# Performance work log

Hardware: AMD Instinct MI355X
Metric: run time of the kernel (lower is better)

Reference implementation:

```python
import jax, jax.numpy as jnp
import numpy as np


def _dplr_scan(q, k, v, a, b, gk, scale=1.0):
    """RWKV-7 DPLR delta-rule recurrence. All inputs [B,H,S,D]; fp32 state."""
    B, H, S, D = q.shape
    Dv = v.shape[-1]
    h0 = jnp.zeros((B, H, D, Dv), dtype=jnp.float32)
    qf = q.astype(jnp.float32) * scale
    kf = k.astype(jnp.float32)
    vf = v.astype(jnp.float32)
    af = a.astype(jnp.float32)
    bf = b.astype(jnp.float32)
    gf = gk.astype(jnp.float32)

    def step(h, xs):
        q_t, k_t, v_t, a_t, b_t, gk_t = xs  # each [B,H,D]
        a_h = jnp.einsum('bhk,bhkv->bhv', a_t, h)
        h = jnp.exp(gk_t)[..., None] * h + b_t[..., None] * a_h[..., None, :] \
            + jnp.einsum('bhk,bhv->bhkv', k_t, v_t)
        o_t = jnp.einsum('bhkv,bhk->bhv', h, q_t)
        return h, o_t

    xs = tuple(jnp.transpose(x, (2, 0, 1, 3)) for x in (qf, kf, vf, af, bf, gf))
    h_final, outs = jax.lax.scan(step, h0, xs)  # outs [S,B,H,Dv]
    return jnp.transpose(outs, (1, 2, 0, 3)).astype(q.dtype), h_final


def setup_inputs() -> dict:
    key = jax.random.key(0)
    B, H, S, D = 2, 32, 1024, 64
    hid = H * D
    ks = jax.random.split(key, 8)
    q = jax.random.normal(ks[0], (B, H, S, D), jnp.float32)
    kk = jax.random.normal(ks[1], (B, H, S, D), jnp.float32)
    kn = kk / jnp.sqrt(jnp.sum(kk * kk, -1, keepdims=True) + 1e-12)  # l2-norm keys
    v = jax.random.normal(ks[2], (B, H, S, D), jnp.float32)
    a = -kn                                                           # a = -kk
    a_scalar = jax.nn.sigmoid(jax.random.normal(ks[3], (B, H, S, D)))
    b = kn * a_scalar                                                 # b = kk * a_scalar
    gk = -0.6 + 0.5 * jax.random.uniform(ks[4], (B, H, S, D))         # log decay < 0
    r_k = jax.random.normal(ks[5], (H, D), jnp.float32) * 0.1
    g = jax.nn.sigmoid(jax.random.normal(ks[6], (B, S, hid), jnp.float32))
    gn_scale = jnp.ones((hid,), jnp.float32)
    gn_bias = jnp.zeros((hid,), jnp.float32)
    return dict(q=q, k=kn, v=v, a=a, b=b, gk=gk, r_k=r_k, g=g,
                gn_scale=gn_scale, gn_bias=gn_bias)


def reference(q, k, v, a, b, gk, r_k, g, gn_scale, gn_bias):
    B, H, S, D = q.shape
    Dv = v.shape[-1]
    eps = 1e-5
    o, _ = _dplr_scan(q, k, v, a, b, gk)          # [B,H,S,Dv]
    o = jnp.transpose(o, (0, 2, 1, 3))             # [B,S,H,Dv]
    # GroupNorm with num_groups = H (per-head normalization over Dv)
    mu = jnp.mean(o, -1, keepdims=True)
    var = jnp.var(o, -1, keepdims=True)
    o = (o - mu) * jax.lax.rsqrt(var + eps)
    o = o * gn_scale.reshape(H, Dv) + gn_bias.reshape(H, Dv)
    o = o.reshape(B, S, H * Dv)
    # output correction: ((r*k*r_k).sum(-1) * v), then gate
    r_ = jnp.transpose(q, (0, 2, 1, 3))            # [B,S,H,D]
    k_ = jnp.transpose(k, (0, 2, 1, 3))
    v_ = jnp.transpose(v, (0, 2, 1, 3))
    corr = jnp.sum(r_ * k_ * r_k[None, None], -1, keepdims=True) * v_
    return (o + corr.reshape(B, S, -1)) * g
```

## Files before the change

### kernel.cpp

```cpp
#include <hip/hip_runtime.h>
#include <hip/hip_bf16.h>

constexpr int Bb = 2, Hh = 32, Ss = 1024, Dd = 64;
constexpr int NBH = Bb * Hh;

template<int SEG, int CH>
__global__ __launch_bounds__(64, 2) void scan_gm(
    const float* __restrict__ qp, const float* __restrict__ kp,
    const float* __restrict__ vp, const float* __restrict__ ap,
    const float* __restrict__ bp, const float* __restrict__ gkp,
    float* __restrict__ Gbuf, float* __restrict__ Mbuf,
    float* __restrict__ zbuf, float* __restrict__ out)
{
    constexpr int NP = Ss / SEG;
    const int lane = (int)threadIdx.x;
    const int bid  = (int)blockIdx.x;
    const int p    = bid & (NP - 1);
    const int bh   = bid / NP;
    const int b    = bh >> 5, hh = bh & (Hh - 1);
    const size_t segbase = (size_t)bid * (SEG * Dd);

    __shared__ float la[CH * 64], lb[CH * 64], lw_[CH * 64];
    __shared__ float lq[CH * 64], lk[CH * 64], lv[CH * 64];

    float h[64], m[64];
#pragma unroll
    for (int j = 0; j < 64; ++j) {
        h[j] = 0.f;
        m[j] = (j == lane) ? 1.f : 0.f;
    }

    for (int c0 = 0; c0 < SEG; c0 += CH) {
        __syncthreads();
        {
            const size_t gb = segbase + (size_t)c0 * 64;
            const float4* a4 = (const float4*)(ap + gb);
            const float4* b4 = (const float4*)(bp + gb);
            const float4* g4 = (const float4*)(gkp + gb);
            const float4* q4 = (const float4*)(qp + gb);
            const float4* k4 = (const float4*)(kp + gb);
            const float4* v4 = (const float4*)(vp + gb);
#pragma unroll
            for (int i = lane; i < CH * 16; i += 64) {
                ((float4*)la)[i] = a4[i];
                ((float4*)lb)[i] = b4[i];
                float4 g = g4[i], e;
                e.x = __expf(g.x); e.y = __expf(g.y);
                e.z = __expf(g.z); e.w = __expf(g.w);
                ((float4*)lw_)[i] = e;
                ((float4*)lq)[i] = q4[i];
                ((float4*)lk)[i] = k4[i];
                ((float4*)lv)[i] = v4[i];
            }
        }
        __syncthreads();

#pragma unroll
        for (int tl = 0; tl < CH; ++tl) {
            const int t = c0 + tl;
            const float4* ar = (const float4*)(la + tl * 64);
            float s0 = 0.f, s1 = 0.f, s2 = 0.f, s3 = 0.f;
            float r0 = 0.f, r1 = 0.f, r2 = 0.f, r3 = 0.f;
#pragma unroll
            for (int jj = 0; jj < 16; ++jj) {
                const float4 a4 = ar[jj];
                s0 = fmaf(a4.x, h[4*jj+0], s0);
                r0 = fmaf(a4.x, m[4*jj+0], r0);
                s1 = fmaf(a4.y, h[4*jj+1], s1);
                r1 = fmaf(a4.y, m[4*jj+1], r1);
                s2 = fmaf(a4.z, h[4*jj+2], s2);
                r2 = fmaf(a4.z, m[4*jj+2], r2);
                s3 = fmaf(a4.w, h[4*jj+3], s3);
                r3 = fmaf(a4.w, m[4*jj+3], r3);
            }
            const float ah = (s0 + s1) + (s2 + s3);
            const float am = (r0 + r1) + (r2 + r3);

            const float u = lv[tl * 64 + lane];
            const float4* br = (const float4*)(lb  + tl * 64);
            const float4* wr = (const float4*)(lw_ + tl * 64);
            const float4* qr = (const float4*)(lq  + tl * 64);
            const float4* kr = (const float4*)(lk  + tl * 64);
            float o0 = 0.f, o1 = 0.f, o2 = 0.f, o3 = 0.f;
            float z0 = 0.f, z1 = 0.f, z2 = 0.f, z3 = 0.f;
#pragma unroll
            for (int jj = 0; jj < 16; ++jj) {
                const float4 b4 = br[jj], k4 = kr[jj], w4 = wr[jj], q4 = qr[jj];
                h[4*jj+0] = fmaf(w4.x, h[4*jj+0], fmaf(b4.x, ah, k4.x * u));
                m[4*jj+0] = fmaf(w4.x, m[4*jj+0], b4.x * am);
                o0 = fmaf(q4.x, h[4*jj+0], o0);
                z0 = fmaf(q4.x, m[4*jj+0], z0);
                h[4*jj+1] = fmaf(w4.y, h[4*jj+1], fmaf(b4.y, ah, k4.y * u));
                m[4*jj+1] = fmaf(w4.y, m[4*jj+1], b4.y * am);
                o1 = fmaf(q4.y, h[4*jj+1], o1);
                z1 = fmaf(q4.y, m[4*jj+1], z1);
                h[4*jj+2] = fmaf(w4.z, h[4*jj+2], fmaf(b4.z, ah, k4.z * u));
                m[4*jj+2] = fmaf(w4.z, m[4*jj+2], b4.z * am);
                o2 = fmaf(q4.z, h[4*jj+2], o2);
                z2 = fmaf(q4.z, m[4*jj+2], z2);
                h[4*jj+3] = fmaf(w4.w, h[4*jj+3], fmaf(b4.w, ah, k4.w * u));
                m[4*jj+3] = fmaf(w4.w, m[4*jj+3], b4.w * am);
                o3 = fmaf(q4.w, h[4*jj+3], o3);
                z3 = fmaf(q4.w, m[4*jj+3], z3);
            }
            const int s = p * SEG + t;
            out[(((size_t)b * Ss + s) * Hh + hh) * Dd + lane] =
                (o0 + o1) + (o2 + o3);
            zbuf[segbase + (size_t)t * 64 + lane] = (z0 + z1) + (z2 + z3);
        }
    }

    float* gd = Gbuf + (size_t)bid * 4096;
    float* md = Mbuf + (size_t)bid * 4096;
#pragma unroll
    for (int j = 0; j < 64; ++j) {
        gd[j * 64 + lane] = h[j];
        md[j * 64 + lane] = m[j];
    }
}

template<int NP>
__global__ __launch_bounds__(256) void combine(
    const float* __restrict__ Mbuf, float* __restrict__ Gbuf)
{
    const int bh  = (int)blockIdx.x & (NBH - 1);
    const int cb  = (int)blockIdx.x >> 6;
    const int c0  = cb * 16;
    const int tid = (int)threadIdx.x;
    const int cl  = tid & 15;
    const int c   = c0 + cl;
    const int rg  = tid >> 4;
    const int r0  = rg * 4;
    const int xorv = (rg & 1) << 2;

    __shared__ float4 Ml[2][1024];
    __shared__ __align__(16) float swT[16][68];

    {
        const float* G0 = Gbuf + (size_t)bh * NP * 4096;
        for (int i = tid; i < 1024; i += 256)
            swT[i & 15][i >> 4] = G0[(i >> 4) * 64 + c0 + (i & 15)];
    }

    float4 mreg[4];
    if (NP > 1) {
        const float4* Mp = (const float4*)(Mbuf + ((size_t)bh * NP + 1) * 4096);
#pragma unroll
        for (int j = 0; j < 4; ++j) mreg[j] = Mp[j * 256 + tid];
    }
    __syncthreads();
#pragma unroll
    for (int j = 0; j < 4; ++j) {
        const int f = j * 256 + tid;
        Ml[0][f ^ ((f >> 4) & 4)] = mreg[j];
    }
    if (NP > 2) {
        const float4* Mp = (const float4*)(Mbuf + ((size_t)bh * NP + 2) * 4096);
#pragma unroll
        for (int j = 0; j < 4; ++j) mreg[j] = Mp[j * 256 + tid];
    }
    __syncthreads();

    for (int p = 1; p < NP; ++p) {
        const int par = (p - 1) & 1;
        float* Gp = Gbuf + ((size_t)bh * NP + p) * 4096;

        float gacc[4];
#pragma unroll
        for (int r = 0; r < 4; ++r) gacc[r] = Gp[(r0 + r) * 64 + c];

        float accA[4] = {0.f, 0.f, 0.f, 0.f};
        float accB[4] = {0.f, 0.f, 0.f, 0.f};
        const float4* swr = (const float4*)&swT[cl][0];
#pragma unroll
        for (int m4 = 0; m4 < 16; ++m4) {
            const float4 s = swr[m4];
            const int ms = m4 ^ xorv;
#pragma unroll
            for (int r = 0; r < 4; ++r) {
                const float4 m = Ml[par][(r0 + r) * 16 + ms];
                accA[r] = fmaf(m.x, s.x, fmaf(m.y, s.y, accA[r]));
                accB[r] = fmaf(m.z, s.z, fmaf(m.w, s.w, accB[r]));
            }
        }
        __syncthreads();

#pragma unroll
        for (int r = 0; r < 4; ++r) {
            const float val = accA[r] + accB[r] + gacc[r];
            swT[cl][r0 + r] = val;
            Gp[(r0 + r) * 64 + c] = val;
        }
        if (p + 1 < NP) {
#pragma unroll
            for (int j = 0; j < 4; ++j) {
                const int f = j * 256 + tid;
                Ml[par ^ 1][f ^ ((f >> 4) & 4)] = mreg[j];
            }
        }
        if (p + 2 < NP) {
            const float4* Mp = (const float4*)(Mbuf + ((size_t)bh * NP + p + 2) * 4096);
#pragma unroll
            for (int j = 0; j < 4; ++j) mreg[j] = Mp[j * 256 + tid];
        }
        __syncthreads();
    }
}

template<int SEG>
__global__ __launch_bounds__(256) void seg_correct(
    const float* __restrict__ Gbuf, const float* __restrict__ zbuf,
    float* __restrict__ out)
{
    constexpr int NP = Ss / SEG;
    const int bid = (int)blockIdx.x;
    const int bh  = bid / (NP - 1);
    const int p   = bid % (NP - 1) + 1;
    const int tid = (int)threadIdx.x;
    const int lane = tid & 63;
    const int w    = tid >> 6;
    const int b = bh >> 5, hh = bh & (Hh - 1);

    __shared__ float SWs[4096];
    __shared__ float zs[SEG * 64];

    const float* sw = Gbuf + ((size_t)bh * NP + p - 1) * 4096;
    const float* zp = zbuf + ((size_t)(bh * NP + p)) * (SEG * 64);
    for (int i = tid; i < 4096; i += 256)
        SWs[i] = sw[i];
    for (int i = tid; i < SEG * 64; i += 256)
        zs[i] = zp[i];
    __syncthreads();

    for (int t = w; t < SEG; t += 4) {
        float a0 = 0.f, a1 = 0.f, a2 = 0.f, a3 = 0.f;
#pragma unroll
        for (int k = 0; k < 64; k += 4) {
            a0 = fmaf(zs[t * 64 + k + 0], SWs[(k + 0) * 64 + lane], a0);
            a1 = fmaf(zs[t * 64 + k + 1], SWs[(k + 1) * 64 + lane], a1);
            a2 = fmaf(zs[t * 64 + k + 2], SWs[(k + 2) * 64 + lane], a2);
            a3 = fmaf(zs[t * 64 + k + 3], SWs[(k + 3) * 64 + lane], a3);
        }
        const int s = p * SEG + t;
        const size_t o = (((size_t)b * Ss + s) * Hh + hh) * Dd + lane;
        out[o] += (a0 + a1) + (a2 + a3);
    }
}

__global__ __launch_bounds__(256) void epilogue(
    const float* __restrict__ qp, const float* __restrict__ kp,
    const float* __restrict__ vp, const float* __restrict__ rk,
    const float* __restrict__ gp, const float* __restrict__ sc,
    const float* __restrict__ bi, float* __restrict__ out)
{
    const int lane = (int)(threadIdx.x & 63u);
    const int gid  = (int)blockIdx.x * 4 + (int)(threadIdx.x >> 6);
    const int hh   = gid & (Hh - 1);
    const int bs   = gid >> 5;
    const int b    = bs >> 10;
    const int s    = bs & (Ss - 1);

    const size_t ioff = ((size_t)(b * Hh + hh) * Ss + s) * Dd + lane;
    const float qv = qp[ioff];
    const float kv = kp[ioff];
    const float vv = vp[ioff];
    const float r  = rk[hh * Dd + lane];

    const size_t goff = (size_t)bs * (Hh * Dd) + hh * Dd + lane;
    const float o = out[goff];

    float s1 = o, s2 = o * o, s3 = qv * kv * r;
#pragma unroll
    for (int m = 32; m >= 1; m >>= 1) {
        s1 += __shfl_xor(s1, m, 64);
        s2 += __shfl_xor(s2, m, 64);
        s3 += __shfl_xor(s3, m, 64);
    }
    const float mu  = s1 * (1.f / 64.f);
    const float var = fmaf(-mu, mu, s2 * (1.f / 64.f));
    const float on  = (o - mu) * rsqrtf(var + 1e-5f);

    out[goff] = (fmaf(on, sc[hh * Dd + lane], bi[hh * Dd + lane]) + s3 * vv) * gp[goff];
}

extern "C" void kernel_launch(void* const* d_in, const int* in_sizes, int n_in,
                              void* d_out, int out_size, void* d_ws, size_t ws_size,
                              hipStream_t stream)
{
    const float* q   = (const float*)d_in[0];
    const float* k   = (const float*)d_in[1];
    const float* v   = (const float*)d_in[2];
    const float* a   = (const float*)d_in[3];
    const float* b   = (const float*)d_in[4];
    const float* gk  = (const float*)d_in[5];
    const float* r_k = (const float*)d_in[6];
    const float* g   = (const float*)d_in[7];
    const float* gns = (const float*)d_in[8];
    const float* gnb = (const float*)d_in[9];
    float* out = (float*)d_out;
    float* ws  = (float*)d_ws;

    const size_t zfl   = (size_t)NBH * Ss * 64;
    const size_t gm32  = (size_t)NBH * 32 * 4096;
    const size_t gm16  = (size_t)NBH * 16 * 4096;
    const size_t need32 = (2 * gm32 + zfl) * sizeof(float);
    const size_t need16 = (2 * gm16 + zfl) * sizeof(float);

    if (ws_size >= need32) {
        float* G = ws;
        float* M = ws + gm32;
        float* Z = ws + 2 * gm32;
        scan_gm<32, 8><<<dim3(NBH * 32), dim3(64), 0, stream>>>(
            q, k, v, a, b, gk, G, M, Z, out);
        combine<32><<<dim3(NBH * 4), dim3(256), 0, stream>>>(M, G);
        seg_correct<32><<<dim3(NBH * 31), dim3(256), 0, stream>>>(G, Z, out);
    } else {
        float* G = ws;
        float* M = ws + gm16;
        float* Z = ws + 2 * gm16;
        scan_gm<64, 16><<<dim3(NBH * 16), dim3(64), 0, stream>>>(
            q, k, v, a, b, gk, G, M, Z, out);
        combine<16><<<dim3(NBH * 4), dim3(256), 0, stream>>>(M, G);
        seg_correct<64><<<dim3(NBH * 15), dim3(256), 0, stream>>>(G, Z, out);
    }

    epilogue<<<dim3(Bb * Ss * Hh / 4), dim3(256), 0, stream>>>(
        q, k, v, r_k, g, gns, gnb, out);
}
```

Before: 195.1 us.

## Pack a, b, q, k to bf16 in LDS and drop block barriers in scan

The scan kernel now rounds a, b, q and k to bf16 and stores them packed two per 32-bit word in shared memory, halving LDS reads for those operands in the inner loops. The decay and v stay in fp32. Both __syncthreads calls are removed, which relies on the block being a single 64-lane wavefront. Launch bounds drop from two waves per SIMD to one, and the dot-product accumulator chains are cut from four to two. This trades accuracy on the state update for fewer LDS reads and fewer instructions.

```diff
diff --git a/kernel.cpp b/kernel.cpp
--- a/kernel.cpp
+++ b/kernel.cpp
@@ -4,8 +4,32 @@
 constexpr int Bb = 2, Hh = 32, Ss = 1024, Dd = 64;
 constexpr int NBH = Bb * Hh;
 
+__device__ __forceinline__ unsigned pk2(float x0, float x1) {
+    const unsigned u0 = __float_as_uint(x0) + 0x8000u;
+    const unsigned u1 = __float_as_uint(x1) + 0x8000u;
+    return (u0 >> 16) | (u1 & 0xffff0000u);
+}
+#define LOF(u) __uint_as_float((u) << 16)
+#define HIF(u) __uint_as_float((u) & 0xffff0000u)
+
+#define ADOT2(au, E)                                            \
+    { const float aL = LOF(au), aH = HIF(au);                   \
+      s0 = fmaf(aL, h[(E)],     s0); r0 = fmaf(aL, m[(E)],     r0); \
+      s1 = fmaf(aH, h[(E) + 1], s1); r1 = fmaf(aH, m[(E) + 1], r1); }
+
+#define STEP2(bu, qu, ku, wA, wB, E)                                    \
+    { const float bL = LOF(bu), bH = HIF(bu);                           \
+      const float qL = LOF(qu), qH = HIF(qu);                           \
+      const float kL = LOF(ku), kH = HIF(ku);                           \
+      h[(E)]     = fmaf(wA, h[(E)],     fmaf(bL, ah, kL * u));          \
+      m[(E)]     = fmaf(wA, m[(E)],     bL * am);                       \
+      o0 = fmaf(qL, h[(E)], o0);     z0 = fmaf(qL, m[(E)], z0);         \
+      h[(E) + 1] = fmaf(wB, h[(E) + 1], fmaf(bH, ah, kH * u));          \
+      m[(E) + 1] = fmaf(wB, m[(E) + 1], bH * am);                       \
+      o1 = fmaf(qH, h[(E) + 1], o1); z1 = fmaf(qH, m[(E) + 1], z1); }
+
 template<int SEG, int CH>
-__global__ __launch_bounds__(64, 2) void scan_gm(
+__global__ __launch_bounds__(64, 1) void scan_gm(
     const float* __restrict__ qp, const float* __restrict__ kp,
     const float* __restrict__ vp, const float* __restrict__ ap,
     const float* __restrict__ bp, const float* __restrict__ gkp,
@@ -20,8 +44,12 @@
     const int b    = bh >> 5, hh = bh & (Hh - 1);
     const size_t segbase = (size_t)bid * (SEG * Dd);
 
-    __shared__ float la[CH * 64], lb[CH * 64], lw_[CH * 64];
-    __shared__ float lq[CH * 64], lk[CH * 64], lv[CH * 64];
+    __shared__ float    lw_[CH * 64];
+    __shared__ float    lv [CH * 64];
+    __shared__ unsigned laP[CH * 32];
+    __shared__ unsigned lbP[CH * 32];
+    __shared__ unsigned lqP[CH * 32];
+    __shared__ unsigned lkP[CH * 32];
 
     float h[64], m[64];
 #pragma unroll
@@ -31,82 +59,70 @@
     }
 
     for (int c0 = 0; c0 < SEG; c0 += CH) {
-        __syncthreads();
         {
             const size_t gb = segbase + (size_t)c0 * 64;
-            const float4* a4 = (const float4*)(ap + gb);
-            const float4* b4 = (const float4*)(bp + gb);
-            const float4* g4 = (const float4*)(gkp + gb);
-            const float4* q4 = (const float4*)(qp + gb);
-            const float4* k4 = (const float4*)(kp + gb);
-            const float4* v4 = (const float4*)(vp + gb);
 #pragma unroll
             for (int i = lane; i < CH * 16; i += 64) {
-                ((float4*)la)[i] = a4[i];
-                ((float4*)lb)[i] = b4[i];
-                float4 g = g4[i], e;
-                e.x = __expf(g.x); e.y = __expf(g.y);
-                e.z = __expf(g.z); e.w = __expf(g.w);
+                const float4 av = ((const float4*)(ap  + gb))[i];
+                const float4 bv = ((const float4*)(bp  + gb))[i];
+                const float4 qv = ((const float4*)(qp  + gb))[i];
+                const float4 kv = ((const float4*)(kp  + gb))[i];
+                const float4 gv = ((const float4*)(gkp + gb))[i];
+                const float4 vv = ((const float4*)(vp  + gb))[i];
+                float4 e;
+                e.x = __expf(gv.x); e.y = __expf(gv.y);
+                e.z = __expf(gv.z); e.w = __expf(gv.w);
                 ((float4*)lw_)[i] = e;
-                ((float4*)lq)[i] = q4[i];
-                ((float4*)lk)[i] = k4[i];
-                ((float4*)lv)[i] = v4[i];
-            }
-        }
-        __syncthreads();
+                ((float4*)lv )[i] = vv;
+                uint2 pa; pa.x = pk2(av.x, av.y); pa.y = pk2(av.z, av.w);
+                uint2 pb; pb.x = pk2(bv.x, bv.y); pb.y = pk2(bv.z, bv.w);
+                uint2 pq; pq.x = pk2(qv.x, qv.y); pq.y = pk2(qv.z, qv.w);
+                uint2 pk_; pk_.x = pk2(kv.x, kv.y); pk_.y = pk2(kv.z, kv.w);
+                ((uint2*)laP)[i] = pa;
+                ((uint2*)lbP)[i] = pb;
+                ((uint2*)lqP)[i] = pq;
+                ((uint2*)lkP)[i] = pk_;
+            }
+        }
 
 #pragma unroll
         for (int tl = 0; tl < CH; ++tl) {
             const int t = c0 + tl;
-            const float4* ar = (const float4*)(la + tl * 64);
-            float s0 = 0.f, s1 = 0.f, s2 = 0.f, s3 = 0.f;
-            float r0 = 0.f, r1 = 0.f, r2 = 0.f, r3 = 0.f;
-#pragma unroll
-            for (int jj = 0; jj < 16; ++jj) {
-                const float4 a4 = ar[jj];
-                s0 = fmaf(a4.x, h[4*jj+0], s0);
-                r0 = fmaf(a4.x, m[4*jj+0], r0);
-                s1 = fmaf(a4.y, h[4*jj+1], s1);
-                r1 = fmaf(a4.y, m[4*jj+1], r1);
-                s2 = fmaf(a4.z, h[4*jj+2], s2);
-                r2 = fmaf(a4.z, m[4*jj+2], r2);
-                s3 = fmaf(a4.w, h[4*jj+3], s3);
-                r3 = fmaf(a4.w, m[4*jj+3], r3);
-            }
-            const float ah = (s0 + s1) + (s2 + s3);
-            const float am = (r0 + r1) + (r2 + r3);
-
+            const uint4* aP = (const uint4*)(laP + tl * 32);
+            float s0 = 0.f, s1 = 0.f, r0 = 0.f, r1 = 0.f;
+#pragma unroll
+            for (int jj = 0; jj < 8; ++jj) {
+                const uint4 ua = aP[jj];
+                const int e = 8 * jj;
+                ADOT2(ua.x, e + 0);
+                ADOT2(ua.y, e + 2);
+                ADOT2(ua.z, e + 4);
+                ADOT2(ua.w, e + 6);
+            }
+            const float ah = s0 + s1;
+            const float am = r0 + r1;
+
+            const uint4*  bP = (const uint4*)(lbP + tl * 32);
+            const uint4*  qP = (const uint4*)(lqP + tl * 32);
+            const uint4*  kP = (const uint4*)(lkP + tl * 32);
+            const float4* wr = (const float4*)(lw_ + tl * 64);
             const float u = lv[tl * 64 + lane];
-            const float4* br = (const float4*)(lb  + tl * 64);
-            const float4* wr = (const float4*)(lw_ + tl * 64);
-            const float4* qr = (const float4*)(lq  + tl * 64);
-            const float4* kr = (const float4*)(lk  + tl * 64);
-            float o0 = 0.f, o1 = 0.f, o2 = 0.f, o3 = 0.f;
-            float z0 = 0.f, z1 = 0.f, z2 = 0.f, z3 = 0.f;
-#pragma unroll
-            for (int jj = 0; jj < 16; ++jj) {
-                const float4 b4 = br[jj], k4 = kr[jj], w4 = wr[jj], q4 = qr[jj];
-                h[4*jj+0] = fmaf(w4.x, h[4*jj+0], fmaf(b4.x, ah, k4.x * u));
-                m[4*jj+0] = fmaf(w4.x, m[4*jj+0], b4.x * am);
-                o0 = fmaf(q4.x, h[4*jj+0], o0);
-                z0 = fmaf(q4.x, m[4*jj+0], z0);
-                h[4*jj+1] = fmaf(w4.y, h[4*jj+1], fmaf(b4.y, ah, k4.y * u));
-                m[4*jj+1] = fmaf(w4.y, m[4*jj+1], b4.y * am);
-                o1 = fmaf(q4.y, h[4*jj+1], o1);
-                z1 = fmaf(q4.y, m[4*jj+1], z1);
-                h[4*jj+2] = fmaf(w4.z, h[4*jj+2], fmaf(b4.z, ah, k4.z * u));
-                m[4*jj+2] = fmaf(w4.z, m[4*jj+2], b4.z * am);
-                o2 = fmaf(q4.z, h[4*jj+2], o2);
-                z2 = fmaf(q4.z, m[4*jj+2], z2);
-                h[4*jj+3] = fmaf(w4.w, h[4*jj+3], fmaf(b4.w, ah, k4.w * u));
-                m[4*jj+3] = fmaf(w4.w, m[4*jj+3], b4.w * am);
-                o3 = fmaf(q4.w, h[4*jj+3], o3);
-                z3 = fmaf(q4.w, m[4*jj+3], z3);
+            float o0 = 0.f, o1 = 0.f, z0 = 0.f, z1 = 0.f;
+#pragma unroll
+            for (int jj = 0; jj < 8; ++jj) {
+                const uint4 ub = bP[jj];
+                const uint4 uq = qP[jj];
+                const uint4 uk = kP[jj];
+                const float4 w0 = wr[2 * jj], w1 = wr[2 * jj + 1];
+                const int e = 8 * jj;
+                STEP2(ub.x, uq.x, uk.x, w0.x, w0.y, e + 0);
+                STEP2(ub.y, uq.y, uk.y, w0.z, w0.w, e + 2);
+                STEP2(ub.z, uq.z, uk.z, w1.x, w1.y, e + 4);
+                STEP2(ub.w, uq.w, uk.w, w1.z, w1.w, e + 6);
             }
             const int s = p * SEG + t;
-            out[(((size_t)b * Ss + s) * Hh + hh) * Dd + lane] =
-                (o0 + o1) + (o2 + o3);
-            zbuf[segbase + (size_t)t * 64 + lane] = (z0 + z1) + (z2 + z3);
+            out[(((size_t)b * Ss + s) * Hh + hh) * Dd + lane] = o0 + o1;
+            zbuf[segbase + (size_t)t * 64 + lane] = z0 + z1;
         }
     }
 
@@ -304,7 +320,7 @@
     const size_t gm32  = (size_t)NBH * 32 * 4096;
     const size_t gm16  = (size_t)NBH * 16 * 4096;
     const size_t need32 = (2 * gm32 + zfl) * sizeof(float);
-    const size_t need16 = (2 * gm16 + zfl) * sizeof(float);
+    (void)need32;
 
     if (ws_size >= need32) {
         float* G = ws;
```

Measured after the change: 260.0 us. 1.33x slower.
